# Kernel optimization log

Hardware: AMD Instinct MI355X
Metric: run time of the kernel (lower is better)

The kernel has to match this reference:

```python
import jax, jax.numpy as jnp
import numpy as np

EPS = 1e-8  # torch.cosine_similarity default eps


def setup_inputs() -> dict:
    key = jax.random.key(0)
    k1, k2 = jax.random.split(key)
    N, D = 2_000_000, 128
    query_embedding = jax.random.normal(k1, (1, D), dtype=jnp.float32)
    index_matrix = jax.random.normal(k2, (N, D), dtype=jnp.float32)
    return {
        "query_embedding": query_embedding,
        "index_matrix": index_matrix,
        "top_k": 5,
    }


def reference(query_embedding, index_matrix, top_k):
    # cosine similarity of [1, D] query against [N, D] memory bank
    # torch.cosine_similarity: dot / max(||q|| * ||m||, eps)
    q = query_embedding[0]                       # [D]
    dots = index_matrix @ q                       # [N]
    q_norm = jnp.sqrt(jnp.sum(q * q))             # scalar
    m_norms = jnp.sqrt(jnp.sum(index_matrix * index_matrix, axis=1))  # [N]
    sims = dots / jnp.maximum(q_norm * m_norms, EPS)                  # [N]
    top_vals, top_idx = jax.lax.top_k(sims, top_k)
    return top_vals, top_idx
```

## Files before the change

### kernel.cpp

```cpp
#include <hip/hip_runtime.h>

#define K 5
#define D 128
#define BLOCK 256
#define NBLOCKS 2048

typedef float vf4 __attribute__((ext_vector_type(4)));

__device__ __forceinline__ void insert_top(float sim, int idx, float bv[K], int bi[K]) {
    if (sim > bv[K - 1]) {
        bv[K - 1] = sim;
        bi[K - 1] = idx;
#pragma unroll
        for (int j = K - 1; j > 0; --j) {
            if (bv[j] > bv[j - 1]) {
                float tv = bv[j]; bv[j] = bv[j - 1]; bv[j - 1] = tv;
                int   ti = bi[j]; bi[j] = bi[j - 1]; bi[j - 1] = ti;
            }
        }
    }
}

extern "C" __global__ void __launch_bounds__(BLOCK)
cossim_topk_pass1(const float* __restrict__ q, const float* __restrict__ M, int N,
                  float* __restrict__ cand_v, int* __restrict__ cand_i) {
    const int tid   = threadIdx.x;
    const int lane  = tid & 63;
    const int wib   = tid >> 6;
    const int wid   = blockIdx.x * (BLOCK / 64) + wib;
    const int nwave = gridDim.x * (BLOCK / 64);
    const int rsub  = lane >> 3;
    const int chunk = lane & 7;

    const vf4* __restrict__ Mv = reinterpret_cast<const vf4*>(M);
    const float4* __restrict__ qf4 = reinterpret_cast<const float4*>(q);

    float4 qf[4];
#pragma unroll
    for (int j = 0; j < 4; ++j) qf[j] = qf4[chunk + j * 8];

    float q2 = 0.f;
#pragma unroll
    for (int j = 0; j < 4; ++j)
        q2 = fmaf(qf[j].x, qf[j].x, fmaf(qf[j].y, qf[j].y,
             fmaf(qf[j].z, qf[j].z, fmaf(qf[j].w, qf[j].w, q2))));
#pragma unroll
    for (int m = 1; m <= 4; m <<= 1) q2 += __shfl_xor(q2, m);
    const float qn = sqrtf(q2);

    float bv[K]; int bi[K];
#pragma unroll
    for (int j = 0; j < K; ++j) { bv[j] = -3.0e38f; bi[j] = 0; }

    const int stride = nwave * 16;
    for (int base = wid * 16; base < N; base += stride) {
        const int rowA = base + rsub;
        const int rowB = base + 8 + rsub;
        const int rcA  = rowA < N ? rowA : N - 1;
        const int rcB  = rowB < N ? rowB : N - 1;
        const size_t rbA = (size_t)rcA * (D / 4);
        const size_t rbB = (size_t)rcB * (D / 4);

        vf4 a[4], b[4];
#pragma unroll
        for (int j = 0; j < 4; ++j) a[j] = __builtin_nontemporal_load(&Mv[rbA + chunk + j * 8]);
#pragma unroll
        for (int j = 0; j < 4; ++j) b[j] = __builtin_nontemporal_load(&Mv[rbB + chunk + j * 8]);

        {
            float dot = 0.f, ss = 0.f;
#pragma unroll
            for (int j = 0; j < 4; ++j) {
                dot = fmaf(a[j].x, qf[j].x, fmaf(a[j].y, qf[j].y,
                      fmaf(a[j].z, qf[j].z, fmaf(a[j].w, qf[j].w, dot))));
                ss  = fmaf(a[j].x, a[j].x,  fmaf(a[j].y, a[j].y,
                      fmaf(a[j].z, a[j].z,  fmaf(a[j].w, a[j].w, ss))));
            }
#pragma unroll
            for (int m = 1; m <= 4; m <<= 1) { dot += __shfl_xor(dot, m); ss += __shfl_xor(ss, m); }
            const float sim = dot / fmaxf(qn * sqrtf(ss), 1e-8f);
            if (rowA < N) insert_top(sim, rowA, bv, bi);
        }
        {
            float dot = 0.f, ss = 0.f;
#pragma unroll
            for (int j = 0; j < 4; ++j) {
                dot = fmaf(b[j].x, qf[j].x, fmaf(b[j].y, qf[j].y,
                      fmaf(b[j].z, qf[j].z, fmaf(b[j].w, qf[j].w, dot))));
                ss  = fmaf(b[j].x, b[j].x,  fmaf(b[j].y, b[j].y,
                      fmaf(b[j].z, b[j].z,  fmaf(b[j].w, b[j].w, ss))));
            }
#pragma unroll
            for (int m = 1; m <= 4; m <<= 1) { dot += __shfl_xor(dot, m); ss += __shfl_xor(ss, m); }
            const float sim = dot / fmaxf(qn * sqrtf(ss), 1e-8f);
            if (rowB < N) insert_top(sim, rowB, bv, bi);
        }
    }

#pragma unroll
    for (int m = 8; m <= 32; m <<= 1) {
        float ov[K]; int oi[K];
#pragma unroll
        for (int j = 0; j < K; ++j) { ov[j] = __shfl_xor(bv[j], m); oi[j] = __shfl_xor(bi[j], m); }
#pragma unroll
        for (int j = 0; j < K; ++j) insert_top(ov[j], oi[j], bv, bi);
    }

    __shared__ float sv[(BLOCK / 64) * K];
    __shared__ int   si[(BLOCK / 64) * K];
    if (lane == 0) {
#pragma unroll
        for (int j = 0; j < K; ++j) { sv[wib * K + j] = bv[j]; si[wib * K + j] = bi[j]; }
    }
    __syncthreads();
    if (tid == 0) {
        float mv[K]; int mi[K];
#pragma unroll
        for (int j = 0; j < K; ++j) { mv[j] = sv[j]; mi[j] = si[j]; }
        for (int c = K; c < (BLOCK / 64) * K; ++c) insert_top(sv[c], si[c], mv, mi);
#pragma unroll
        for (int j = 0; j < K; ++j) {
            cand_v[blockIdx.x * K + j] = mv[j];
            cand_i[blockIdx.x * K + j] = mi[j];
        }
    }
}

extern "C" __global__ void __launch_bounds__(256)
cossim_topk_pass2(const float* __restrict__ cand_v, const int* __restrict__ cand_i,
                  int ncand, float* __restrict__ out) {
    const int tid = threadIdx.x;
    float bv[K]; int bi[K];
#pragma unroll
    for (int j = 0; j < K; ++j) { bv[j] = -3.0e38f; bi[j] = 0; }

    for (int c = tid; c < ncand; c += 256) insert_top(cand_v[c], cand_i[c], bv, bi);

#pragma unroll
    for (int m = 1; m <= 32; m <<= 1) {
        float ov[K]; int oi[K];
#pragma unroll
        for (int j = 0; j < K; ++j) { ov[j] = __shfl_xor(bv[j], m); oi[j] = __shfl_xor(bi[j], m); }
#pragma unroll
        for (int j = 0; j < K; ++j) insert_top(ov[j], oi[j], bv, bi);
    }

    __shared__ float sv[4 * K];
    __shared__ int   si[4 * K];
    if ((tid & 63) == 0) {
        const int w = tid >> 6;
#pragma unroll
        for (int j = 0; j < K; ++j) { sv[w * K + j] = bv[j]; si[w * K + j] = bi[j]; }
    }
    __syncthreads();

    if (tid == 0) {
        float mv[K]; int mi[K];
#pragma unroll
        for (int j = 0; j < K; ++j) { mv[j] = sv[j]; mi[j] = si[j]; }
        for (int c = K; c < 4 * K; ++c) insert_top(sv[c], si[c], mv, mi);
#pragma unroll
        for (int j = 0; j < K; ++j) {
            out[j]     = mv[j];
            out[K + j] = (float)mi[j];
        }
    }
}

extern "C" void kernel_launch(void* const* d_in, const int* in_sizes, int n_in,
                              void* d_out, int out_size, void* d_ws, size_t ws_size,
                              hipStream_t stream) {
    const float* q = (const float*)d_in[0];
    const float* M = (const float*)d_in[1];
    const int N = in_sizes[1] / D;

    int nb = NBLOCKS;
    const size_t need = (size_t)nb * K * (sizeof(float) + sizeof(int));
    if (need > ws_size) nb = (int)(ws_size / (K * (sizeof(float) + sizeof(int))));

    float* cand_v = (float*)d_ws;
    int*   cand_i = (int*)((char*)d_ws + (size_t)nb * K * sizeof(float));

    hipLaunchKernelGGL(cossim_topk_pass1, dim3(nb), dim3(BLOCK), 0, stream,
                       q, M, N, cand_v, cand_i);
    hipLaunchKernelGGL(cossim_topk_pass2, dim3(1), dim3(256), 0, stream,
                       cand_v, cand_i, nb * K, (float*)d_out);
}
```

Before: 184.7 us.

## Fuse top-k passes via last-block atomic ticket and halve grid size

Merges the second reduction kernel into the first: each block bumps an atomic ticket after writing its candidates, and the last block to arrive runs the final top-k merge. The grid also shrinks from 2048 to 1024 blocks, which halves the candidate count. This drops a kernel launch and its gap but adds a memset launch and threadfences. The smaller grid may lower memory-level parallelism on a bandwidth-bound 1 GB scan.

```diff
diff --git a/kernel.cpp b/kernel.cpp
--- a/kernel.cpp
+++ b/kernel.cpp
@@ -3,7 +3,7 @@
 #define K 5
 #define D 128
 #define BLOCK 256
-#define NBLOCKS 2048
+#define NBLOCKS 1024
 
 typedef float vf4 __attribute__((ext_vector_type(4)));
 
@@ -22,8 +22,9 @@
 }
 
 extern "C" __global__ void __launch_bounds__(BLOCK)
-cossim_topk_pass1(const float* __restrict__ q, const float* __restrict__ M, int N,
-                  float* __restrict__ cand_v, int* __restrict__ cand_i) {
+cossim_topk_fused(const float* __restrict__ q, const float* __restrict__ M, int N,
+                  float* __restrict__ cand_v, int* __restrict__ cand_i,
+                  int* __restrict__ ticket, float* __restrict__ out) {
     const int tid   = threadIdx.x;
     const int lane  = tid & 63;
     const int wib   = tid >> 6;
@@ -124,41 +125,46 @@
             cand_i[blockIdx.x * K + j] = mi[j];
         }
     }
-}
 
-extern "C" __global__ void __launch_bounds__(256)
-cossim_topk_pass2(const float* __restrict__ cand_v, const int* __restrict__ cand_i,
-                  int ncand, float* __restrict__ out) {
-    const int tid = threadIdx.x;
-    float bv[K]; int bi[K];
+    __shared__ int is_last;
+    __threadfence();
+    if (tid == 0) {
+        const int prev = atomicAdd(ticket, 1);
+        is_last = (prev == (int)gridDim.x - 1);
+    }
+    __syncthreads();
+    if (!is_last) return;
+
+    __threadfence();
+    const volatile float* vv = cand_v;
+    const volatile int*   vi = cand_i;
+    const int ncand = (int)gridDim.x * K;
+
+    float fv[K]; int fi[K];
 #pragma unroll
-    for (int j = 0; j < K; ++j) { bv[j] = -3.0e38f; bi[j] = 0; }
-
-    for (int c = tid; c < ncand; c += 256) insert_top(cand_v[c], cand_i[c], bv, bi);
+    for (int j = 0; j < K; ++j) { fv[j] = -3.0e38f; fi[j] = 0; }
+    for (int c = tid; c < ncand; c += BLOCK) insert_top(vv[c], vi[c], fv, fi);
 
 #pragma unroll
     for (int m = 1; m <= 32; m <<= 1) {
         float ov[K]; int oi[K];
 #pragma unroll
-        for (int j = 0; j < K; ++j) { ov[j] = __shfl_xor(bv[j], m); oi[j] = __shfl_xor(bi[j], m); }
+        for (int j = 0; j < K; ++j) { ov[j] = __shfl_xor(fv[j], m); oi[j] = __shfl_xor(fi[j], m); }
 #pragma unroll
-        for (int j = 0; j < K; ++j) insert_top(ov[j], oi[j], bv, bi);
+        for (int j = 0; j < K; ++j) insert_top(ov[j], oi[j], fv, fi);
     }
 
-    __shared__ float sv[4 * K];
-    __shared__ int   si[4 * K];
-    if ((tid & 63) == 0) {
-        const int w = tid >> 6;
+    __syncthreads();
+    if (lane == 0) {
 #pragma unroll
-        for (int j = 0; j < K; ++j) { sv[w * K + j] = bv[j]; si[w * K + j] = bi[j]; }
+        for (int j = 0; j < K; ++j) { sv[wib * K + j] = fv[j]; si[wib * K + j] = fi[j]; }
     }
     __syncthreads();
-
     if (tid == 0) {
         float mv[K]; int mi[K];
 #pragma unroll
         for (int j = 0; j < K; ++j) { mv[j] = sv[j]; mi[j] = si[j]; }
-        for (int c = K; c < 4 * K; ++c) insert_top(sv[c], si[c], mv, mi);
+        for (int c = K; c < (BLOCK / 64) * K; ++c) insert_top(sv[c], si[c], mv, mi);
 #pragma unroll
         for (int j = 0; j < K; ++j) {
             out[j]     = mv[j];
@@ -175,14 +181,16 @@
     const int N = in_sizes[1] / D;
 
     int nb = NBLOCKS;
-    const size_t need = (size_t)nb * K * (sizeof(float) + sizeof(int));
-    if (need > ws_size) nb = (int)(ws_size / (K * (sizeof(float) + sizeof(int))));
+    const size_t per_blk = K * (sizeof(float) + sizeof(int));
+    if ((size_t)nb * per_blk + sizeof(int) > ws_size)
+        nb = (int)((ws_size - sizeof(int)) / per_blk);
 
     float* cand_v = (float*)d_ws;
     int*   cand_i = (int*)((char*)d_ws + (size_t)nb * K * sizeof(float));
+    int*   ticket = (int*)((char*)d_ws + (size_t)nb * per_blk);
 
-    hipLaunchKernelGGL(cossim_topk_pass1, dim3(nb), dim3(BLOCK), 0, stream,
-                       q, M, N, cand_v, cand_i);
-    hipLaunchKernelGGL(cossim_topk_pass2, dim3(1), dim3(256), 0, stream,
-                       cand_v, cand_i, nb * K, (float*)d_out);
+    hipMemsetAsync(ticket, 0, sizeof(int), stream);
+
+    hipLaunchKernelGGL(cossim_topk_fused, dim3(nb), dim3(BLOCK), 0, stream,
+                       q, M, N, cand_v, cand_i, ticket, (float*)d_out);
 }
```

Measured after the change: 374.2 us. +102.6%, slower.
